# Performance work log

Hardware: AMD Instinct MI355X
Metric: run time of the kernel (lower is better)

Reference implementation:

```python
import jax, jax.numpy as jnp
import numpy as np

B, N, D = 32, 512, 1024
H, DH = 8, 64
INNER = H * DH          # 512
PROJ = 512
MID = (D + PROJ) // 2   # 768
EPS = 1e-5


def _ln(x, gamma):
    # F.layer_norm over last dim, beta is a zeros buffer
    m = jnp.mean(x, axis=-1, keepdims=True)
    v = jnp.var(x, axis=-1, keepdims=True)
    return (x - m) * jax.lax.rsqrt(v + EPS) * gamma


def setup_inputs() -> dict:
    key = jax.random.key(0)
    ks = jax.random.split(key, 12)
    s = 0.02
    return {
        "x": jax.random.normal(ks[0], (B, N, D), dtype=jnp.float32),
        "pos_encoding": jax.random.normal(ks[1], (1, N, D), dtype=jnp.float32),
        "queries": jax.random.normal(ks[2], (N, D), dtype=jnp.float32),
        "ln_q_g": jnp.ones((D,), dtype=jnp.float32),
        "ln_ctx_g": jnp.ones((D,), dtype=jnp.float32),
        "Wq": jax.random.normal(ks[3], (D, INNER), dtype=jnp.float32) * s,
        "Wkv": jax.random.normal(ks[4], (D, 2 * DH), dtype=jnp.float32) * s,
        "Wout": jax.random.normal(ks[5], (INNER, D), dtype=jnp.float32) * s,
        "ln_post_g": jnp.ones((D,), dtype=jnp.float32),
        "W1": jax.random.normal(ks[6], (D, MID), dtype=jnp.float32) * s,
        "b1": jnp.zeros((MID,), dtype=jnp.float32),
        "W2": jax.random.normal(ks[7], (MID, PROJ), dtype=jnp.float32) * s,
        "b2": jnp.zeros((PROJ,), dtype=jnp.float32),
        "zero_masks": jnp.ones((B, N), dtype=jnp.int32),  # unused (masking commented out in source)
    }


def reference(x, pos_encoding, queries, ln_q_g, ln_ctx_g, Wq, Wkv, Wout,
              ln_post_g, W1, b1, W2, b2, zero_masks):
    scale = DH ** -0.5
    x = x.astype(jnp.float32) + pos_encoding                   # [B,N,D]
    q_in = jnp.broadcast_to(queries[None], (B, N, D))          # learned queries per batch

    # CrossAttention (norm_context=True, parallel_ff=False)
    qn = _ln(q_in, ln_q_g)
    ctx = _ln(x, ln_ctx_g)
    q = (qn @ Wq).reshape(B, N, H, DH).transpose(0, 2, 1, 3) * scale   # [B,H,N,DH]
    kv = ctx @ Wkv                                                     # [B,N,2*DH]
    k, v = kv[..., :DH], kv[..., DH:]                                  # shared across heads (MQA)
    sim = jnp.einsum('bhid,bjd->bhij', q, k)                           # [B,H,N,N]
    attn = jax.nn.softmax(sim, axis=-1)                                # max-subtract stable
    out = jnp.einsum('bhij,bjd->bhid', attn, v)                        # [B,H,N,DH]
    out = out.transpose(0, 2, 1, 3).reshape(B, N, INNER) @ Wout        # [B,N,D]

    out = _ln(out, ln_post_g)
    emb = jnp.mean(out, axis=1)                                        # [B,D] video embedding
    pred = jax.nn.gelu(emb @ W1 + b1, approximate=False) @ W2 + b2     # [B,PROJ]
    return pred
```

## Files before the change

### kernel.cpp

```cpp
#include <hip/hip_runtime.h>
#include <cmath>

#define Bz 32
#define Nz 512
#define Dz 1024
#define Hz 8
#define DHz 64
#define INNERz 512
#define PROJz 512
#define MIDz 768
#define EPSz 1e-5f

typedef unsigned short u16;
typedef unsigned int u32;
typedef __attribute__((ext_vector_type(8))) short short8v;
typedef __attribute__((ext_vector_type(8))) unsigned short ushort8v;
typedef __attribute__((ext_vector_type(4))) unsigned short ushort4v;
typedef __attribute__((ext_vector_type(4))) float f32x4;

__device__ __forceinline__ u16 f2bf(float x) {
  unsigned u = __float_as_uint(x);
  unsigned r = u + 0x7fff + ((u >> 16) & 1);
  return (u16)(r >> 16);
}
__device__ __forceinline__ float bf2f(u16 u) {
  return __uint_as_float(((unsigned)u) << 16);
}

__global__ __launch_bounds__(256) void k_prepw(
    const float* __restrict__ Wkv, const float* __restrict__ Wq,
    const float* __restrict__ g_ctx, const float* __restrict__ g_q,
    u16* __restrict__ WkvTg, u16* __restrict__ WqTg,
    float* __restrict__ cskv4, float* __restrict__ csq4) {
  __shared__ float part[64][4];
  const int t = threadIdx.x;
  const int blk = blockIdx.x;
  const int jg = blk >> 2, quarter = blk & 3;
  const bool isq = jg >= 2;
  const int jbase = isq ? (jg - 2) * 64 : jg * 64;
  const int j = jbase + (t & 63);
  const int dsub = t >> 6;
  const float* W = isq ? Wq : Wkv;
  const int ld = isq ? 512 : 128;
  const float* g = isq ? g_q : g_ctx;
  const float scale = isq ? 0.125f : 1.f;
  u16* WT = isq ? WqTg : WkvTg;
  float partial = 0.f;
  const int d0beg = quarter * 256 + dsub * 64;
  for (int d0 = d0beg; d0 < d0beg + 64; d0 += 2) {
    const float v0 = scale * g[d0] * W[(size_t)d0 * ld + j];
    const float v1 = scale * g[d0 + 1] * W[(size_t)(d0 + 1) * ld + j];
    partial += v0 + v1;
    *(u32*)(WT + (size_t)j * Dz + d0) = (u32)f2bf(v0) | ((u32)f2bf(v1) << 16);
  }
  part[t & 63][dsub] = partial;
  __syncthreads();
  if (t < 64)
    (isq ? csq4 : cskv4)[(jbase + t) * 4 + quarter] =
        part[t][0] + part[t][1] + part[t][2] + part[t][3];
}

#define LOADB2(dst, kk)                                                        \
  {                                                                            \
    _Pragma("unroll") for (int u_ = 0; u_ < 4; ++u_)                           \
    _Pragma("unroll") for (int cf_ = 0; cf_ < 2; ++cf_)                        \
        dst[u_][cf_] =                                                         \
            *(const short8v*)(Bp + (size_t)cf_ * 16 * Dz + (kk) + u_ * 32);    \
  }

__global__ __launch_bounds__(256) void k_qproj(
    const float* __restrict__ queries, const u16* __restrict__ WT,
    const float* __restrict__ cs4, u16* __restrict__ qbuf) {
  __shared__ u16 hbuf[16 * 1024];
  __shared__ float mm[16], rr[16];
  char* hb = (char*)hbuf;
  const int t = threadIdx.x;
  {
    const int r = t >> 4, c16 = t & 15;
    const long grow = (long)blockIdx.x * 16 + r;
    const float* xr = queries + grow * Dz;
    float s = 0.f, ss = 0.f;
    const int swz = (r & 7) << 4;
#pragma unroll
    for (int i = 0; i < 16; ++i) {
      const int col = c16 * 4 + i * 64;
      const float4 v = *(const float4*)(xr + col);
      s += (v.x + v.y) + (v.z + v.w);
      ss += (v.x * v.x + v.y * v.y) + (v.z * v.z + v.w * v.w);
      uint2 pk;
      pk.x = (u32)f2bf(v.x) | ((u32)f2bf(v.y) << 16);
      pk.y = (u32)f2bf(v.z) | ((u32)f2bf(v.w) << 16);
      *(uint2*)(hb + ((r * 2048 + col * 2) ^ swz)) = pk;
    }
#pragma unroll
    for (int off = 1; off <= 8; off <<= 1) { s += __shfl_xor(s, off); ss += __shfl_xor(ss, off); }
    const float mean = s * (1.f / Dz);
    const float rstd = rsqrtf(ss * (1.f / Dz) - mean * mean + EPSz);
    if (c16 == 0) { mm[r] = mean; rr[r] = rstd; }
  }
  __syncthreads();
  const int w = t >> 6, l = t & 63;
  const int lr = l & 15, lk = l >> 4;
  const int c0 = blockIdx.y * 128 + w * 32;
  f32x4 acc[2];
  acc[0] = {0.f, 0.f, 0.f, 0.f};
  acc[1] = {0.f, 0.f, 0.f, 0.f};
  const int aswz = (lr & 7) << 4;
  const u16* Bp = WT + (size_t)(c0 + lr) * Dz + lk * 8;
  short8v bcur[4][2], bnxt[4][2];
  LOADB2(bcur, 0);
#pragma unroll
  for (int k0 = 0; k0 < Dz; k0 += 128) {
    if (k0 + 128 < Dz) LOADB2(bnxt, k0 + 128);
#pragma unroll
    for (int u = 0; u < 4; ++u) {
      const int kk = (k0 + u * 32 + lk * 8) * 2;
      const short8v a = *(const short8v*)(hb + ((lr * 2048 + kk) ^ aswz));
      acc[0] = __builtin_amdgcn_mfma_f32_16x16x32_bf16(a, bcur[u][0], acc[0], 0, 0, 0);
      acc[1] = __builtin_amdgcn_mfma_f32_16x16x32_bf16(a, bcur[u][1], acc[1], 0, 0, 0);
    }
    if (k0 + 128 < Dz) {
#pragma unroll
      for (int u = 0; u < 4; ++u) {
        bcur[u][0] = bnxt[u][0];
        bcur[u][1] = bnxt[u][1];
      }
    }
  }
  const long base = (long)blockIdx.x * 16;
#pragma unroll
  for (int cf = 0; cf < 2; ++cf) {
    const int col = c0 + cf * 16 + lr;
    const float c = cs4[col * 4] + cs4[col * 4 + 1] + cs4[col * 4 + 2] + cs4[col * 4 + 3];
#pragma unroll
    for (int q = 0; q < 4; ++q) {
      const int row = lk * 4 + q;
      qbuf[(size_t)(base + row) * INNERz + col] = f2bf(rr[row] * (acc[cf][q] - mm[row] * c));
    }
  }
}

__global__ __launch_bounds__(256) void k_ctxkv(
    const float* __restrict__ x, const float* __restrict__ pos,
    const u16* __restrict__ WT, const float* __restrict__ cs4,
    u16* __restrict__ kb, u16* __restrict__ vT) {
  __shared__ u16 hbuf[32 * 1024];
  __shared__ float mm[32], rrs[32];
  char* hb = (char*)hbuf;
  const int t = threadIdx.x;
  {
    const int r2 = t >> 4, c16 = t & 15;
#pragma unroll
    for (int half = 0; half < 2; ++half) {
      const int r = r2 + half * 16;
      const long grow = (long)blockIdx.x * 32 + r;
      const int n = (int)(grow & (Nz - 1));
      const float* xr = x + grow * Dz;
      const float* pr = pos + (size_t)n * Dz;
      float s = 0.f, ss = 0.f;
      const int swz = (r & 7) << 4;
#pragma unroll
      for (int i = 0; i < 16; ++i) {
        const int col = c16 * 4 + i * 64;
        float4 v = *(const float4*)(xr + col);
        const float4 p = *(const float4*)(pr + col);
        v.x += p.x; v.y += p.y; v.z += p.z; v.w += p.w;
        s += (v.x + v.y) + (v.z + v.w);
        ss += (v.x * v.x + v.y * v.y) + (v.z * v.z + v.w * v.w);
        uint2 pk;
        pk.x = (u32)f2bf(v.x) | ((u32)f2bf(v.y) << 16);
        pk.y = (u32)f2bf(v.z) | ((u32)f2bf(v.w) << 16);
        *(uint2*)(hb + ((r * 2048 + col * 2) ^ swz)) = pk;
      }
#pragma unroll
      for (int off = 1; off <= 8; off <<= 1) { s += __shfl_xor(s, off); ss += __shfl_xor(ss, off); }
      const float mean = s * (1.f / Dz);
      const float rstd = rsqrtf(ss * (1.f / Dz) - mean * mean + EPSz);
      if (c16 == 0) { mm[r] = mean; rrs[r] = rstd; }
    }
  }
  __syncthreads();
  const int w = t >> 6, l = t & 63;
  const int lr = l & 15, lk = l >> 4;
  const int c0 = w * 32;
  f32x4 acc[2][2];
#pragma unroll
  for (int rf = 0; rf < 2; ++rf)
#pragma unroll
    for (int cf = 0; cf < 2; ++cf) acc[rf][cf] = {0.f, 0.f, 0.f, 0.f};
  const int aswz = (lr & 7) << 4;
  const u16* Bp = WT + (size_t)(c0 + lr) * Dz + lk * 8;
  short8v bcur[4][2], bnxt[4][2];
  LOADB2(bcur, 0);
#pragma unroll
  for (int k0 = 0; k0 < Dz; k0 += 128) {
    if (k0 + 128 < Dz) LOADB2(bnxt, k0 + 128);
#pragma unroll
    for (int u = 0; u < 4; ++u) {
      const int kk = (k0 + u * 32 + lk * 8) * 2;
      const short8v a0 = *(const short8v*)(hb + ((lr * 2048 + kk) ^ aswz));
      const short8v a1 = *(const short8v*)(hb + (((lr + 16) * 2048 + kk) ^ aswz));
      acc[0][0] = __builtin_amdgcn_mfma_f32_16x16x32_bf16(a0, bcur[u][0], acc[0][0], 0, 0, 0);
      acc[0][1] = __builtin_amdgcn_mfma_f32_16x16x32_bf16(a0, bcur[u][1], acc[0][1], 0, 0, 0);
      acc[1][0] = __builtin_amdgcn_mfma_f32_16x16x32_bf16(a1, bcur[u][0], acc[1][0], 0, 0, 0);
      acc[1][1] = __builtin_amdgcn_mfma_f32_16x16x32_bf16(a1, bcur[u][1], acc[1][1], 0, 0, 0);
    }
    if (k0 + 128 < Dz) {
#pragma unroll
      for (int u = 0; u < 4; ++u) {
        bcur[u][0] = bnxt[u][0];
        bcur[u][1] = bnxt[u][1];
      }
    }
  }
  const long base = (long)blockIdx.x * 32;
  const int bb = (int)(base >> 9), nb0 = (int)(base & (Nz - 1));
#pragma unroll
  for (int rf = 0; rf < 2; ++rf)
#pragma unroll
    for (int cf = 0; cf < 2; ++cf) {
      const int col = c0 + cf * 16 + lr;
      const float c = cs4[col * 4] + cs4[col * 4 + 1] + cs4[col * 4 + 2] + cs4[col * 4 + 3];
      if (col < 64) {
#pragma unroll
        for (int q = 0; q < 4; ++q) {
          const int row = rf * 16 + lk * 4 + q;
          kb[(size_t)(base + row) * DHz + col] = f2bf(rrs[row] * (acc[rf][cf][q] - mm[row] * c));
        }
      } else {
        ushort4v pk;
#pragma unroll
        for (int q = 0; q < 4; ++q) {
          const int row = rf * 16 + lk * 4 + q;
          pk[q] = f2bf(rrs[row] * (acc[rf][cf][q] - mm[row] * c));
        }
        *(ushort4v*)(vT + ((size_t)bb * DHz + (col - 64)) * Nz + nb0 + rf * 16 + lk * 4) = pk;
      }
    }
}

__global__ __launch_bounds__(256) void k_attn(
    const u16* __restrict__ qb, const u16* __restrict__ kb,
    const u16* __restrict__ vT, u16* __restrict__ ao) {
  __shared__ u16 Ks[2][4096];
  __shared__ u16 Vs[2][4096];
  __shared__ u16 plds[4][1024];
  const int t = threadIdx.x;
  const int w = t >> 6, l = t & 63;
  const int lr = l & 15, lk = l >> 4;
  const int m0 = blockIdx.x * 64 + w * 16;
  const int h = blockIdx.y, b = blockIdx.z;
  const u16* qrow = qb + (size_t)(m0 + lr) * INNERz + h * DHz + lk * 8;
  const short8v aq0 = *(const short8v*)qrow;
  const short8v aq1 = *(const short8v*)(qrow + 32);
  const u16* kbB = kb + (size_t)b * Nz * DHz;
  const u16* vTB = vT + (size_t)b * DHz * Nz;
  char* pw = (char*)&plds[w][0];
  const int swz = (lr & 7) << 4;

  const int srow = w * 16 + (l >> 3);
  const int schunk = (l & 7) ^ (l >> 3);

#define STAGE(bufi, j0v)                                                              \
  {                                                                                   \
    _Pragma("unroll") for (int c = 0; c < 2; ++c) {                                   \
      __builtin_amdgcn_global_load_lds(                                               \
          (const __attribute__((address_space(1))) u32*)(const void*)(                \
              kbB + (size_t)((j0v) + srow + c * 8) * DHz + schunk * 8),               \
          (__attribute__((address_space(3))) u32*)(void*)(&Ks[bufi][0] + w * 1024 + c * 512), \
          16, 0, 0);                                                                  \
      __builtin_amdgcn_global_load_lds(                                               \
          (const __attribute__((address_space(1))) u32*)(const void*)(                \
              vTB + (size_t)(srow + c * 8) * Nz + (j0v) + schunk * 8),                \
          (__attribute__((address_space(3))) u32*)(void*)(&Vs[bufi][0] + w * 1024 + c * 512), \
          16, 0, 0);                                                                  \
    }                                                                                 \
  }

  f32x4 oacc[4];
#pragma unroll
  for (int dn = 0; dn < 4; ++dn) oacc[dn] = {0.f, 0.f, 0.f, 0.f};
  float lsum = 0.f;

  int buf = 0;
  STAGE(0, 0);
  asm volatile("s_waitcnt vmcnt(0)" ::: "memory");
  __builtin_amdgcn_s_barrier();
  asm volatile("" ::: "memory");

  for (int tt = 0; tt < 8; ++tt) {
    if (tt < 7) STAGE(buf ^ 1, (tt + 1) * 64);
    asm volatile("" ::: "memory");
    const char* Kb = (const char*)&Ks[buf][0];
    const char* Vb = (const char*)&Vs[buf][0];
    f32x4 sfr[4];
#pragma unroll
    for (int jn = 0; jn < 4; ++jn) {
      const int rbase = jn * 2048 + lr * 128;
      const short8v bk0 = *(const short8v*)(Kb + rbase + ((lk * 16) ^ swz));
      const short8v bk1 = *(const short8v*)(Kb + rbase + ((64 + lk * 16) ^ swz));
      f32x4 c = {0.f, 0.f, 0.f, 0.f};
      c = __builtin_amdgcn_mfma_f32_16x16x32_bf16(bk0, aq0, c, 0, 0, 0);
      c = __builtin_amdgcn_mfma_f32_16x16x32_bf16(bk1, aq1, c, 0, 0, 0);
      sfr[jn] = c;
    }
    float ps = 0.f;
#pragma unroll
    for (int jn = 0; jn < 4; ++jn) {
      const float e0 = __expf(sfr[jn][0]);
      const float e1 = __expf(sfr[jn][1]);
      const float e2 = __expf(sfr[jn][2]);
      const float e3 = __expf(sfr[jn][3]);
      ps += (e0 + e1) + (e2 + e3);
      const u32 p01 = (u32)f2bf(e0) | ((u32)f2bf(e1) << 16);
      const u32 p23 = (u32)f2bf(e2) | ((u32)f2bf(e3) << 16);
      const int pbase = (lr * 128 + jn * 32 + lk * 8) ^ swz;
      *(u32*)(pw + pbase) = p01;
      *(u32*)(pw + pbase + 4) = p23;
    }
    lsum += ps;
    const short8v pa0 = *(const short8v*)(pw + ((lr * 128 + lk * 16) ^ swz));
    const short8v pa1 = *(const short8v*)(pw + ((lr * 128 + 64 + lk * 16) ^ swz));
#pragma unroll
    for (int dn = 0; dn < 4; ++dn) {
      const int rbase = dn * 2048 + lr * 128;
      const short8v bv0 = *(const short8v*)(Vb + rbase + ((lk * 16) ^ swz));
      const short8v bv1 = *(const short8v*)(Vb + rbase + ((64 + lk * 16) ^ swz));
      f32x4 o = oacc[dn];
      o = __builtin_amdgcn_mfma_f32_16x16x32_bf16(pa0, bv0, o, 0, 0, 0);
      o = __builtin_amdgcn_mfma_f32_16x16x32_bf16(pa1, bv1, o, 0, 0, 0);
      oacc[dn] = o;
    }
    asm volatile("" ::: "memory");
    if (tt < 7) asm volatile("s_waitcnt vmcnt(0)" ::: "memory");
    __builtin_amdgcn_s_barrier();
    asm volatile("" ::: "memory");
    buf ^= 1;
  }
#undef STAGE
  lsum += __shfl_xor(lsum, 16);
  lsum += __shfl_xor(lsum, 32);
  float rinv[4];
#pragma unroll
  for (int r = 0; r < 4; ++r) rinv[r] = 1.f / __shfl(lsum, lk * 4 + r, 64);
#pragma unroll
  for (int dn = 0; dn < 4; ++dn)
#pragma unroll
    for (int r = 0; r < 4; ++r) {
      const int row = m0 + lk * 4 + r;
      ao[((size_t)b * Nz + row) * INNERz + h * DHz + dn * 16 + lr] =
          f2bf(oacc[dn][r] * rinv[r]);
    }
}

__global__ __launch_bounds__(256) void k_prep(const float* __restrict__ Wout,
                                              u16* __restrict__ WoutT) {
  __shared__ float sm[32][33];
  const int t = threadIdx.x;
  const int n0 = blockIdx.x * 32, k0 = blockIdx.y * 32;
  {
    const int kk = t >> 3, nn = (t & 7) * 4;
    const float4 v = *reinterpret_cast<const float4*>(Wout + (size_t)(k0 + kk) * Dz + n0 + nn);
    sm[kk][nn] = v.x; sm[kk][nn + 1] = v.y; sm[kk][nn + 2] = v.z; sm[kk][nn + 3] = v.w;
  }
  __syncthreads();
  const int nn = t >> 3, kk = (t & 7) * 4;
  ushort4v pk;
#pragma unroll
  for (int j = 0; j < 4; ++j) pk[j] = f2bf(sm[kk + j][nn]);
  *reinterpret_cast<ushort4v*>(WoutT + (size_t)(n0 + nn) * INNERz + k0 + kk) = pk;
}

__global__ __launch_bounds__(256) void k_wgemm(
    const u16* __restrict__ A, const u16* __restrict__ BT, u16* __restrict__ C) {
  __shared__ u16 As[128 * 64];
  __shared__ u16 Bs[128 * 64];
  const int t = threadIdx.x;
  const int w = t >> 6, l = t & 63;
  const int m0 = blockIdx.y * 128, n0 = blockIdx.x * 128;
  const int wr = w >> 1, wc = w & 1;
  const int lr = l & 15, lk = l >> 4;

  f32x4 acc[4][4];
#pragma unroll
  for (int mt = 0; mt < 4; ++mt)
#pragma unroll
    for (int nt = 0; nt < 4; ++nt) acc[mt][nt] = {0.f, 0.f, 0.f, 0.f};

  for (int k0 = 0; k0 < INNERz; k0 += 64) {
#pragma unroll
    for (int c = 0; c < 4; ++c) {
      const int rowblk = w * 32 + c * 8;
      const int row = rowblk + (l >> 3);
      const int kb16 = (l & 7) * 8;
      __builtin_amdgcn_global_load_lds(
          (const __attribute__((address_space(1))) unsigned int*)(const void*)(
              A + (size_t)(m0 + row) * INNERz + k0 + kb16),
          (__attribute__((address_space(3))) unsigned int*)(void*)(As + rowblk * 64),
          16, 0, 0);
      __builtin_amdgcn_global_load_lds(
          (const __attribute__((address_space(1))) unsigned int*)(const void*)(
              BT + (size_t)(n0 + row) * INNERz + k0 + kb16),
          (__attribute__((address_space(3))) unsigned int*)(void*)(Bs + rowblk * 64),
          16, 0, 0);
    }
    __syncthreads();
#pragma unroll
    for (int ks = 0; ks < 2; ++ks) {
      short8v af[4], bf[4];
#pragma unroll
      for (int mt = 0; mt < 4; ++mt)
        af[mt] = *reinterpret_cast<const short8v*>(As + (wr * 64 + mt * 16 + lr) * 64 + ks * 32 + lk * 8);
#pragma unroll
      for (int nt = 0; nt < 4; ++nt)
        bf[nt] = *reinterpret_cast<const short8v*>(Bs + (wc * 64 + nt * 16 + lr) * 64 + ks * 32 + lk * 8);
#pragma unroll
      for (int mt = 0; mt < 4; ++mt)
#pragma unroll
        for (int nt = 0; nt < 4; ++nt)
          acc[mt][nt] = __builtin_amdgcn_mfma_f32_16x16x32_bf16(af[mt], bf[nt], acc[mt][nt], 0, 0, 0);
    }
    __syncthreads();
  }
#pragma unroll
  for (int mt = 0; mt < 4; ++mt)
#pragma unroll
    for (int nt = 0; nt < 4; ++nt) {
      const f32x4 a = acc[mt][nt];
#pragma unroll
      for (int r = 0; r < 4; ++r) {
        const size_t row = (size_t)m0 + wr * 64 + mt * 16 + lk * 4 + r;
        C[row * Dz + n0 + wc * 64 + nt * 16 + lr] = f2bf(a[r]);
      }
    }
}

__global__ __launch_bounds__(256) void k_lnmean(
    const u16* __restrict__ out1, float* __restrict__ pbuf) {
  const int t = threadIdx.x;
  const int w = t >> 6, l = t & 63;
  const long row0 = (long)blockIdx.x * 64 + w * 16;
  float acc[16];
#pragma unroll
  for (int j = 0; j < 16; ++j) acc[j] = 0.f;
  for (int rr = 0; rr < 16; ++rr) {
    const u16* rowp = out1 + (size_t)(row0 + rr) * Dz + l * 16;
    const ushort8v u0 = *(const ushort8v*)(rowp);
    const ushort8v u1 = *(const ushort8v*)(rowp + 8);
    float v[16];
#pragma unroll
    for (int j = 0; j < 8; ++j) { v[j] = bf2f(u0[j]); v[8 + j] = bf2f(u1[j]); }
    float s = 0.f, q = 0.f;
#pragma unroll
    for (int j = 0; j < 16; ++j) { s += v[j]; q += v[j] * v[j]; }
#pragma unroll
    for (int off = 1; off <= 32; off <<= 1) { s += __shfl_xor(s, off); q += __shfl_xor(q, off); }
    const float mean = s * (1.f / Dz);
    const float rstd = rsqrtf(q * (1.f / Dz) - mean * mean + EPSz);
#pragma unroll
    for (int j = 0; j < 16; ++j) acc[j] += (v[j] - mean) * rstd;
  }
  float* dst = pbuf + ((size_t)blockIdx.x * 4 + w) * Dz + l * 16;
#pragma unroll
  for (int j = 0; j < 4; ++j)
    *(float4*)(dst + j * 4) =
        make_float4(acc[j * 4], acc[j * 4 + 1], acc[j * 4 + 2], acc[j * 4 + 3]);
}

__global__ __launch_bounds__(256) void k_embred(
    const float* __restrict__ pbuf, const float* __restrict__ g,
    float* __restrict__ emb) {
  const int b = blockIdx.x, t = threadIdx.x;
  const float invN = 1.f / (float)Nz;
  const float* src = pbuf + (size_t)b * 32 * Dz + t * 4;
  float4 s = {0.f, 0.f, 0.f, 0.f};
#pragma unroll 8
  for (int sub = 0; sub < 32; ++sub) {
    const float4 v = *(const float4*)(src + (size_t)sub * Dz);
    s.x += v.x; s.y += v.y; s.z += v.z; s.w += v.w;
  }
  const float4 gv = *(const float4*)(g + t * 4);
  float4 o;
  o.x = s.x * gv.x * invN;
  o.y = s.y * gv.y * invN;
  o.z = s.z * gv.z * invN;
  o.w = s.w * gv.w * invN;
  *(float4*)(emb + (size_t)b * Dz + t * 4) = o;
}

__global__ __launch_bounds__(256) void k_mlp1(
    const float* __restrict__ emb, const float* __restrict__ W1,
    const float* __restrict__ b1, float* __restrict__ mid) {
  __shared__ float e[Dz];
  __shared__ float red[4][64];
  const int b = blockIdx.y, t = threadIdx.x;
  const int col0 = blockIdx.x * 64;
  *reinterpret_cast<float4*>(&e[t * 4]) =
      *reinterpret_cast<const float4*>(emb + (size_t)b * Dz + t * 4);
  __syncthreads();
  const int q = t >> 6, j = t & 63;
  float acc = 0.f;
  const float* W = W1 + (size_t)(q * 256) * MIDz + col0 + j;
#pragma unroll 8
  for (int k = 0; k < 256; ++k) acc += e[q * 256 + k] * W[(size_t)k * MIDz];
  red[q][j] = acc;
  __syncthreads();
  if (t < 64) {
    const float s = red[0][t] + red[1][t] + red[2][t] + red[3][t] + b1[col0 + t];
    mid[(size_t)b * MIDz + col0 + t] = 0.5f * s * (1.f + erff(s * 0.7071067811865475f));
  }
}

__global__ __launch_bounds__(256) void k_mlp2(
    const float* __restrict__ mid, const float* __restrict__ W2,
    const float* __restrict__ b2, float* __restrict__ out) {
  __shared__ float e[MIDz];
  __shared__ float red[4][64];
  const int b = blockIdx.y, t = threadIdx.x;
  const int col0 = blockIdx.x * 64;
  if (t < MIDz / 4)
    *reinterpret_cast<float4*>(&e[t * 4]) =
        *reinterpret_cast<const float4*>(mid + (size_t)b * MIDz + t * 4);
  __syncthreads();
  const int q = t >> 6, j = t & 63;
  float acc = 0.f;
  const float* W = W2 + (size_t)(q * 192) * PROJz + col0 + j;
#pragma unroll 8
  for (int k = 0; k < 192; ++k) acc += e[q * 192 + k] * W[(size_t)k * PROJz];
  red[q][j] = acc;
  __syncthreads();
  if (t < 64)
    out[(size_t)b * PROJz + col0 + t] =
        red[0][t] + red[1][t] + red[2][t] + red[3][t] + b2[col0 + t];
}

extern "C" void kernel_launch(void* const* d_in, const int* in_sizes, int n_in,
                              void* d_out, int out_size, void* d_ws, size_t ws_size,
                              hipStream_t stream) {
  const float* x         = (const float*)d_in[0];
  const float* pos       = (const float*)d_in[1];
  const float* queries   = (const float*)d_in[2];
  const float* ln_q_g    = (const float*)d_in[3];
  const float* ln_ctx_g  = (const float*)d_in[4];
  const float* Wq        = (const float*)d_in[5];
  const float* Wkv       = (const float*)d_in[6];
  const float* Wout      = (const float*)d_in[7];
  const float* ln_post_g = (const float*)d_in[8];
  const float* W1        = (const float*)d_in[9];
  const float* b1        = (const float*)d_in[10];
  const float* W2        = (const float*)d_in[11];
  const float* b2        = (const float*)d_in[12];
  float* out = (float*)d_out;

  char* wsb = (char*)d_ws;
  float* emb   = (float*)wsb;
  float* mid   = (float*)(wsb + 131072);
  u16*   WoutT = (u16*)(wsb + 229376);
  u16*   aobf  = (u16*)(wsb + 1277952);
  float* pbuf  = (float*)(wsb + 1277952);
  u16*   out1  = (u16*)(wsb + 18055168);
  u16*   WkvTg = (u16*)(wsb + 18055168);
  u16*   WqTg  = (u16*)(wsb + 18317312);
  float* cskv4 = (float*)(wsb + 19365888);
  float* csq4  = (float*)(wsb + 19367936);
  u16*   qbbf  = (u16*)(wsb + 19376128);
  u16*   kbbf  = (u16*)(wsb + 19900416);
  u16*   vTbf  = (u16*)(wsb + 21997568);

  k_prepw<<<40, 256, 0, stream>>>(Wkv, Wq, ln_ctx_g, ln_q_g, WkvTg, WqTg, cskv4, csq4);
  k_prep<<<dim3(Dz / 32, INNERz / 32), 256, 0, stream>>>(Wout, WoutT);
  k_qproj<<<dim3(Nz / 16, 4), 256, 0, stream>>>(queries, WqTg, csq4, qbbf);
  k_ctxkv<<<(Bz * Nz) / 32, 256, 0, stream>>>(x, pos, WkvTg, cskv4, kbbf, vTbf);
  k_attn<<<dim3(Nz / 64, Hz, Bz), 256, 0, stream>>>(qbbf, kbbf, vTbf, aobf);
  k_wgemm<<<dim3(Dz / 128, (Bz * Nz) / 128), 256, 0, stream>>>(aobf, WoutT, out1);
  k_lnmean<<<(Bz * Nz) / 64, 256, 0, stream>>>(out1, pbuf);
  k_embred<<<Bz, 256, 0, stream>>>(pbuf, ln_post_g, emb);
  k_mlp1<<<dim3(MIDz / 64, Bz), 256, 0, stream>>>(emb, W1, b1, mid);
  k_mlp2<<<dim3(PROJz / 64, Bz), 256, 0, stream>>>(mid, W2, b2, out);
}
```

Measured before the change: 165.4 us.

## Use native exp2 with folded log2e, packed bf16 convert, smaller ctx-KV tiles

Folds log2(e) into the query weight scale so the attention softmax can call the hardware v_exp_f32 (base-2) directly instead of __expf. It also packs two probabilities into bf16 with one v_cvt_pk_bf16_f32 instruction rather than manual rounding. Separately, k_ctxkv now processes 16 rows per block instead of 32, halving LDS use and doubling the grid for more occupancy and parallelism. The price is that each block re-reads the same weight B-operand over twice as many blocks, and the hardware convert may round slightly differently.

```diff
diff --git a/kernel.cpp b/kernel.cpp
--- a/kernel.cpp
+++ b/kernel.cpp
@@ -26,6 +26,16 @@
 __device__ __forceinline__ float bf2f(u16 u) {
   return __uint_as_float(((unsigned)u) << 16);
 }
+__device__ __forceinline__ float fexp2(float x) {
+  float r;
+  asm("v_exp_f32 %0, %1" : "=v"(r) : "v"(x));
+  return r;
+}
+__device__ __forceinline__ u32 cvtpk(float lo, float hi) {
+  u32 r;
+  asm("v_cvt_pk_bf16_f32 %0, %1, %2" : "=v"(r) : "v"(lo), "v"(hi));
+  return r;
+}
 
 __global__ __launch_bounds__(256) void k_prepw(
     const float* __restrict__ Wkv, const float* __restrict__ Wq,
@@ -43,7 +53,7 @@
   const float* W = isq ? Wq : Wkv;
   const int ld = isq ? 512 : 128;
   const float* g = isq ? g_q : g_ctx;
-  const float scale = isq ? 0.125f : 1.f;
+  const float scale = isq ? 0.125f * 1.4426950408889634f : 1.f;
   u16* WT = isq ? WqTg : WkvTg;
   float partial = 0.f;
   const int d0beg = quarter * 256 + dsub * 64;
@@ -144,50 +154,44 @@
     const float* __restrict__ x, const float* __restrict__ pos,
     const u16* __restrict__ WT, const float* __restrict__ cs4,
     u16* __restrict__ kb, u16* __restrict__ vT) {
-  __shared__ u16 hbuf[32 * 1024];
-  __shared__ float mm[32], rrs[32];
+  __shared__ u16 hbuf[16 * 1024];
+  __shared__ float mm[16], rrs[16];
   char* hb = (char*)hbuf;
   const int t = threadIdx.x;
   {
-    const int r2 = t >> 4, c16 = t & 15;
-#pragma unroll
-    for (int half = 0; half < 2; ++half) {
-      const int r = r2 + half * 16;
-      const long grow = (long)blockIdx.x * 32 + r;
-      const int n = (int)(grow & (Nz - 1));
-      const float* xr = x + grow * Dz;
-      const float* pr = pos + (size_t)n * Dz;
-      float s = 0.f, ss = 0.f;
-      const int swz = (r & 7) << 4;
-#pragma unroll
-      for (int i = 0; i < 16; ++i) {
-        const int col = c16 * 4 + i * 64;
-        float4 v = *(const float4*)(xr + col);
-        const float4 p = *(const float4*)(pr + col);
-        v.x += p.x; v.y += p.y; v.z += p.z; v.w += p.w;
-        s += (v.x + v.y) + (v.z + v.w);
-        ss += (v.x * v.x + v.y * v.y) + (v.z * v.z + v.w * v.w);
-        uint2 pk;
-        pk.x = (u32)f2bf(v.x) | ((u32)f2bf(v.y) << 16);
-        pk.y = (u32)f2bf(v.z) | ((u32)f2bf(v.w) << 16);
-        *(uint2*)(hb + ((r * 2048 + col * 2) ^ swz)) = pk;
-      }
-#pragma unroll
-      for (int off = 1; off <= 8; off <<= 1) { s += __shfl_xor(s, off); ss += __shfl_xor(ss, off); }
-      const float mean = s * (1.f / Dz);
-      const float rstd = rsqrtf(ss * (1.f / Dz) - mean * mean + EPSz);
-      if (c16 == 0) { mm[r] = mean; rrs[r] = rstd; }
-    }
+    const int r = t >> 4, c16 = t & 15;
+    const long grow = (long)blockIdx.x * 16 + r;
+    const int n = (int)(grow & (Nz - 1));
+    const float* xr = x + grow * Dz;
+    const float* pr = pos + (size_t)n * Dz;
+    float s = 0.f, ss = 0.f;
+    const int swz = (r & 7) << 4;
+#pragma unroll
+    for (int i = 0; i < 16; ++i) {
+      const int col = c16 * 4 + i * 64;
+      float4 v = *(const float4*)(xr + col);
+      const float4 p = *(const float4*)(pr + col);
+      v.x += p.x; v.y += p.y; v.z += p.z; v.w += p.w;
+      s += (v.x + v.y) + (v.z + v.w);
+      ss += (v.x * v.x + v.y * v.y) + (v.z * v.z + v.w * v.w);
+      uint2 pk;
+      pk.x = (u32)f2bf(v.x) | ((u32)f2bf(v.y) << 16);
+      pk.y = (u32)f2bf(v.z) | ((u32)f2bf(v.w) << 16);
+      *(uint2*)(hb + ((r * 2048 + col * 2) ^ swz)) = pk;
+    }
+#pragma unroll
+    for (int off = 1; off <= 8; off <<= 1) { s += __shfl_xor(s, off); ss += __shfl_xor(ss, off); }
+    const float mean = s * (1.f / Dz);
+    const float rstd = rsqrtf(ss * (1.f / Dz) - mean * mean + EPSz);
+    if (c16 == 0) { mm[r] = mean; rrs[r] = rstd; }
   }
   __syncthreads();
   const int w = t >> 6, l = t & 63;
   const int lr = l & 15, lk = l >> 4;
   const int c0 = w * 32;
-  f32x4 acc[2][2];
-#pragma unroll
-  for (int rf = 0; rf < 2; ++rf)
-#pragma unroll
-    for (int cf = 0; cf < 2; ++cf) acc[rf][cf] = {0.f, 0.f, 0.f, 0.f};
+  f32x4 acc[2];
+  acc[0] = {0.f, 0.f, 0.f, 0.f};
+  acc[1] = {0.f, 0.f, 0.f, 0.f};
   const int aswz = (lr & 7) << 4;
   const u16* Bp = WT + (size_t)(c0 + lr) * Dz + lk * 8;
   short8v bcur[4][2], bnxt[4][2];
@@ -198,12 +202,9 @@
 #pragma unroll
     for (int u = 0; u < 4; ++u) {
       const int kk = (k0 + u * 32 + lk * 8) * 2;
-      const short8v a0 = *(const short8v*)(hb + ((lr * 2048 + kk) ^ aswz));
-      const short8v a1 = *(const short8v*)(hb + (((lr + 16) * 2048 + kk) ^ aswz));
-      acc[0][0] = __builtin_amdgcn_mfma_f32_16x16x32_bf16(a0, bcur[u][0], acc[0][0], 0, 0, 0);
-      acc[0][1] = __builtin_amdgcn_mfma_f32_16x16x32_bf16(a0, bcur[u][1], acc[0][1], 0, 0, 0);
-      acc[1][0] = __builtin_amdgcn_mfma_f32_16x16x32_bf16(a1, bcur[u][0], acc[1][0], 0, 0, 0);
-      acc[1][1] = __builtin_amdgcn_mfma_f32_16x16x32_bf16(a1, bcur[u][1], acc[1][1], 0, 0, 0);
+      const short8v a = *(const short8v*)(hb + ((lr * 2048 + kk) ^ aswz));
+      acc[0] = __builtin_amdgcn_mfma_f32_16x16x32_bf16(a, bcur[u][0], acc[0], 0, 0, 0);
+      acc[1] = __builtin_amdgcn_mfma_f32_16x16x32_bf16(a, bcur[u][1], acc[1], 0, 0, 0);
     }
     if (k0 + 128 < Dz) {
 #pragma unroll
@@ -213,30 +214,28 @@
       }
     }
   }
-  const long base = (long)blockIdx.x * 32;
+  const long base = (long)blockIdx.x * 16;
   const int bb = (int)(base >> 9), nb0 = (int)(base & (Nz - 1));
 #pragma unroll
-  for (int rf = 0; rf < 2; ++rf)
-#pragma unroll
-    for (int cf = 0; cf < 2; ++cf) {
-      const int col = c0 + cf * 16 + lr;
-      const float c = cs4[col * 4] + cs4[col * 4 + 1] + cs4[col * 4 + 2] + cs4[col * 4 + 3];
-      if (col < 64) {
-#pragma unroll
-        for (int q = 0; q < 4; ++q) {
-          const int row = rf * 16 + lk * 4 + q;
-          kb[(size_t)(base + row) * DHz + col] = f2bf(rrs[row] * (acc[rf][cf][q] - mm[row] * c));
-        }
-      } else {
-        ushort4v pk;
-#pragma unroll
-        for (int q = 0; q < 4; ++q) {
-          const int row = rf * 16 + lk * 4 + q;
-          pk[q] = f2bf(rrs[row] * (acc[rf][cf][q] - mm[row] * c));
-        }
-        *(ushort4v*)(vT + ((size_t)bb * DHz + (col - 64)) * Nz + nb0 + rf * 16 + lk * 4) = pk;
+  for (int cf = 0; cf < 2; ++cf) {
+    const int col = c0 + cf * 16 + lr;
+    const float c = cs4[col * 4] + cs4[col * 4 + 1] + cs4[col * 4 + 2] + cs4[col * 4 + 3];
+    if (col < 64) {
+#pragma unroll
+      for (int q = 0; q < 4; ++q) {
+        const int row = lk * 4 + q;
+        kb[(size_t)(base + row) * DHz + col] = f2bf(rrs[row] * (acc[cf][q] - mm[row] * c));
       }
-    }
+    } else {
+      ushort4v pk;
+#pragma unroll
+      for (int q = 0; q < 4; ++q) {
+        const int row = lk * 4 + q;
+        pk[q] = f2bf(rrs[row] * (acc[cf][q] - mm[row] * c));
+      }
+      *(ushort4v*)(vT + ((size_t)bb * DHz + (col - 64)) * Nz + nb0 + lk * 4) = pk;
+    }
+  }
 }
 
 __global__ __launch_bounds__(256) void k_attn(
@@ -307,13 +306,13 @@
     float ps = 0.f;
 #pragma unroll
     for (int jn = 0; jn < 4; ++jn) {
-      const float e0 = __expf(sfr[jn][0]);
-      const float e1 = __expf(sfr[jn][1]);
-      const float e2 = __expf(sfr[jn][2]);
-      const float e3 = __expf(sfr[jn][3]);
+      const float e0 = fexp2(sfr[jn][0]);
+      const float e1 = fexp2(sfr[jn][1]);
+      const float e2 = fexp2(sfr[jn][2]);
+      const float e3 = fexp2(sfr[jn][3]);
       ps += (e0 + e1) + (e2 + e3);
-      const u32 p01 = (u32)f2bf(e0) | ((u32)f2bf(e1) << 16);
-      const u32 p23 = (u32)f2bf(e2) | ((u32)f2bf(e3) << 16);
+      const u32 p01 = cvtpk(e0, e1);
+      const u32 p23 = cvtpk(e2, e3);
       const int pbase = (lr * 128 + jn * 32 + lk * 8) ^ swz;
       *(u32*)(pw + pbase) = p01;
       *(u32*)(pw + pbase + 4) = p23;
@@ -570,7 +569,7 @@
   k_prepw<<<40, 256, 0, stream>>>(Wkv, Wq, ln_ctx_g, ln_q_g, WkvTg, WqTg, cskv4, csq4);
   k_prep<<<dim3(Dz / 32, INNERz / 32), 256, 0, stream>>>(Wout, WoutT);
   k_qproj<<<dim3(Nz / 16, 4), 256, 0, stream>>>(queries, WqTg, csq4, qbbf);
-  k_ctxkv<<<(Bz * Nz) / 32, 256, 0, stream>>>(x, pos, WkvTg, cskv4, kbbf, vTbf);
+  k_ctxkv<<<(Bz * Nz) / 16, 256, 0, stream>>>(x, pos, WkvTg, cskv4, kbbf, vTbf);
   k_attn<<<dim3(Nz / 64, Hz, Bz), 256, 0, stream>>>(qbbf, kbbf, vTbf, aobf);
   k_wgemm<<<dim3(Dz / 128, (Bz * Nz) / 128), 256, 0, stream>>>(aobf, WoutT, out1);
   k_lnmean<<<(Bz * Nz) / 64, 256, 0, stream>>>(out1, pbuf);
```

After: 174.0 us. 1.05x slower.
